# Kernel tuning notes

Hardware: AMD Instinct MI355X
Metric: run time of the kernel (lower is better)

Reference implementation:

```python
import jax, jax.numpy as jnp
import numpy as np

N_NODES = 100000
N_EDGES = 1600000
NODE_IN = 6
EDGE_IN = 4
HID = 128


def _glorot(key, shape):
    fan_in, fan_out = shape[0], shape[1]
    lim = (6.0 / (fan_in + fan_out)) ** 0.5
    return jax.random.uniform(key, shape, jnp.float32, -lim, lim)


def setup_inputs() -> dict:
    key = jax.random.key(0)
    ks = jax.random.split(key, 16)
    x = jax.random.normal(ks[0], (N_NODES, NODE_IN), jnp.float32)
    edge_index = jax.random.randint(ks[1], (2, N_EDGES), 0, N_NODES, jnp.int64)
    edge_attr = jax.random.normal(ks[2], (N_EDGES, EDGE_IN), jnp.float32)
    # SAGEConv params: out = x @ W_root + mean_neigh @ W_neigh + b
    params = {
        "w1_root": _glorot(ks[3], (NODE_IN, HID)),
        "w1_neigh": _glorot(ks[4], (NODE_IN, HID)),
        "b1": jnp.zeros((HID,), jnp.float32),
        "w2_root": _glorot(ks[5], (HID, HID)),
        "w2_neigh": _glorot(ks[6], (HID, HID)),
        "b2": jnp.zeros((HID,), jnp.float32),
        "w_e1": _glorot(ks[7], (2 * HID + EDGE_IN, HID)),
        "b_e1": jnp.zeros((HID,), jnp.float32),
        "w_e2": _glorot(ks[8], (HID, HID // 2)),
        "b_e2": jnp.zeros((HID // 2,), jnp.float32),
        "w_e3": _glorot(ks[9], (HID // 2, 1)),
        "b_e3": jnp.zeros((1,), jnp.float32),
    }
    return {"x": x, "edge_index": edge_index, "edge_attr": edge_attr, **params}


def _sage(x, src, dst, w_root, w_neigh, b):
    # mean aggregation of source features into destination nodes
    agg = jax.ops.segment_sum(x[src], dst, num_segments=N_NODES)
    cnt = jax.ops.segment_sum(jnp.ones((src.shape[0], 1), x.dtype), dst, num_segments=N_NODES)
    mean = agg / jnp.maximum(cnt, 1.0)
    return x @ w_root + mean @ w_neigh + b


def reference(x, edge_index, edge_attr,
              w1_root, w1_neigh, b1, w2_root, w2_neigh, b2,
              w_e1, b_e1, w_e2, b_e2, w_e3, b_e3):
    src, dst = edge_index[0], edge_index[1]
    h = jax.nn.relu(_sage(x, src, dst, w1_root, w1_neigh, b1))
    # dropout is identity in eval mode
    h = jax.nn.relu(_sage(h, src, dst, w2_root, w2_neigh, b2))
    # per-edge representation: [h[src], h[dst], edge_attr] -> MLP -> scalar
    e = jnp.concatenate([h[src], h[dst], edge_attr], axis=-1)  # [E, 2H+Ein]
    e = jax.nn.relu(e @ w_e1 + b_e1)
    e = jax.nn.relu(e @ w_e2 + b_e2)
    out = (e @ w_e3 + b_e3).squeeze(-1)  # [E]
    return out
```

## Files before the change

kernel.cpp:

```cpp
#include <hip/hip_runtime.h>
#include <hip/hip_bf16.h>
#include <stdint.h>


typedef unsigned short u16;
typedef short bf16x8 __attribute__((ext_vector_type(8)));
typedef float f32x4 __attribute__((ext_vector_type(4)));
typedef float f32x2 __attribute__((ext_vector_type(2)));

#define NMASK 0x1FFFF

__device__ __forceinline__ u16 f2b(float f) {
  unsigned u = __builtin_bit_cast(unsigned, f);
  u = u + 0x7fffu + ((u >> 16) & 1u);
  return (u16)(u >> 16);
}
__device__ __forceinline__ float bflo(unsigned u) {
  return __builtin_bit_cast(float, u << 16);
}
__device__ __forceinline__ float bfhi(unsigned u) {
  return __builtin_bit_cast(float, u & 0xffff0000u);
}
__device__ __forceinline__ f32x2 unpk2(unsigned u) {
  return (f32x2){bflo(u), bfhi(u)};
}
__device__ __forceinline__ unsigned pack2bf(float a, float b) {
  unsigned ua = __builtin_bit_cast(unsigned, a);
  unsigned ub = __builtin_bit_cast(unsigned, b);
  ua = ua + 0x7fffu + ((ua >> 16) & 1u);
  ub = ub + 0x7fffu + ((ub >> 16) & 1u);
  return (ua >> 16) | (ub & 0xffff0000u);
}
__device__ __forceinline__ unsigned packrn(f32x2 f) {
  __hip_bfloat162 h = __float22bfloat162_rn(make_float2(f.x, f.y));
  unsigned r;
  __builtin_memcpy(&r, &h, 4);
  return r;
}

__global__ void hist_kernel(const int* __restrict__ ei, int* __restrict__ cnt,
                            int E) {
  int e = blockIdx.x * blockDim.x + threadIdx.x;
  if (e < E) atomicAdd(&cnt[ei[E + e]], 1);
}

__global__ void scan_block_sums(const int* __restrict__ cnt,
                                int* __restrict__ partial, int N) {
  __shared__ int red[256];
  int t = threadIdx.x;
  int n = blockIdx.x * 256 + t;
  red[t] = (n < N) ? cnt[n] : 0;
  __syncthreads();
  for (int off = 128; off; off >>= 1) {
    if (t < off) red[t] += red[t + off];
    __syncthreads();
  }
  if (t == 0) partial[blockIdx.x] = red[0];
}

__global__ void scan_partials(int* __restrict__ partial,
                              int* __restrict__ rowptr, int NBLK, int E,
                              int N) {
  __shared__ int sc[512];
  int t = threadIdx.x;
  int v = (t < NBLK) ? partial[t] : 0;
  sc[t] = v;
  __syncthreads();
  for (int off = 1; off < 512; off <<= 1) {
    int a = (t >= off) ? sc[t - off] : 0;
    __syncthreads();
    sc[t] += a;
    __syncthreads();
  }
  if (t < NBLK) partial[t] = sc[t] - v;
  if (t == 0) rowptr[N] = E;
}

__global__ void scan_final(const int* __restrict__ partial,
                           int* __restrict__ cursor, int* __restrict__ rowptr,
                           int N) {
  __shared__ int sc[256];
  int t = threadIdx.x;
  int n = blockIdx.x * 256 + t;
  int v = (n < N) ? cursor[n] : 0;
  sc[t] = v;
  __syncthreads();
  for (int off = 1; off < 256; off <<= 1) {
    int a = (t >= off) ? sc[t - off] : 0;
    __syncthreads();
    sc[t] += a;
    __syncthreads();
  }
  int excl = partial[blockIdx.x] + sc[t] - v;
  if (n < N) {
    rowptr[n] = excl;
    cursor[n] = excl;
  }
}

__global__ void scatter_rec(const int* __restrict__ ei,
                            const float* __restrict__ attr,
                            int* __restrict__ cursor, uint4* __restrict__ rec,
                            unsigned* __restrict__ src4, int E) {
  int e = blockIdx.x * blockDim.x + threadIdx.x;
  if (e >= E) return;
  int s = ei[e];
  int d = ei[E + e];
  float4 a4 = *(const float4*)(attr + (size_t)e * 4);
  int pos = atomicAdd(&cursor[d], 1);
  uint4 r;
  r.x = (unsigned)s | ((unsigned)(d & 0x7FFF) << 17);
  r.y = ((unsigned)d >> 15) | ((unsigned)e << 2);
  r.z = pack2bf(a4.x, a4.y);
  r.w = pack2bf(a4.z, a4.w);
  rec[pos] = r;
  src4[pos] = (unsigned)s;
}

__global__ void pack_weights(const float* __restrict__ w2_root,
                             const float* __restrict__ w2_neigh,
                             const float* __restrict__ w_e1,
                             const float* __restrict__ w_e2,
                             const float* __restrict__ b_e1,
                             u16* __restrict__ B2f, u16* __restrict__ WSDf,
                             u16* __restrict__ W2f, float* __restrict__ pbias) {
  int t = blockIdx.x * 256 + threadIdx.x;
  if (t < 32768) {
    int j = t & 7, lane = (t >> 3) & 63, nt = (t >> 9) & 7, kt = t >> 12;
    int k = kt * 32 + (lane >> 4) * 8 + j;
    int n = nt * 16 + (lane & 15);
    float v = (k < 128) ? w2_root[k * 128 + n] : w2_neigh[(k - 128) * 128 + n];
    B2f[t] = f2b(v);
  } else if (t < 65536) {
    int t2 = t - 32768;
    int j = t2 & 7, lane = (t2 >> 3) & 63, nt = (t2 >> 9) & 15, kt = t2 >> 13;
    int k = kt * 32 + (lane >> 4) * 8 + j;
    int n = nt * 16 + (lane & 15);
    float v = (n < 128) ? w_e1[k * 128 + n] : w_e1[(128 + k) * 128 + (n - 128)];
    WSDf[t2] = f2b(v);
  } else if (t < 73728) {
    int t2 = t - 65536;
    int j = t2 & 7, lane = (t2 >> 3) & 63, nt = (t2 >> 9) & 3, kt = t2 >> 11;
    int k = kt * 32 + (lane >> 4) * 8 + j;
    int n = nt * 16 + (lane & 15);
    W2f[t2] = f2b(w_e2[k * 64 + n]);
  } else if (t < 73984) {
    int n = t - 73728;
    pbias[n] = (n < 128) ? 0.0f : b_e1[n - 128];
  }
}

__global__ __launch_bounds__(256) void agg1_kernel(
    const float* __restrict__ x, const int* __restrict__ rowptr,
    const unsigned* __restrict__ src4, float* __restrict__ mean1, int N) {
  int n = blockIdx.x * 4 + (threadIdx.x >> 6);
  if (n >= N) return;
  int lane = threadIdx.x & 63;
  int g = lane >> 3;
  int c = lane & 7;
  int beg = rowptr[n], end = rowptr[n + 1];
  float a = 0.0f;
  if (c < 6) {
    int idx[4];
#pragma unroll
    for (int j = 0; j < 4; j++) {
      int ii = beg + g + j * 8;
      idx[j] = (ii < end) ? (int)src4[ii] : -1;
    }
    float v[4];
#pragma unroll
    for (int j = 0; j < 4; j++)
      v[j] = x[(size_t)(idx[j] < 0 ? 0 : idx[j]) * 6 + c];
#pragma unroll
    for (int j = 0; j < 4; j++)
      if (idx[j] >= 0) a += v[j];
    for (int ii = beg + g + 32; ii < end; ii += 8) {
      a += x[(size_t)src4[ii] * 6 + c];
    }
  }
  a += __shfl_xor(a, 8, 64);
  a += __shfl_xor(a, 16, 64);
  a += __shfl_xor(a, 32, 64);
  if (g == 0 && c < 6)
    mean1[(size_t)n * 6 + c] = a / (float)max(end - beg, 1);
}

__global__ __launch_bounds__(256) void dense1_kernel(
    const float* __restrict__ x, const float* __restrict__ mean1,
    const float* __restrict__ w_root, const float* __restrict__ w_neigh,
    const float* __restrict__ b, u16* __restrict__ cat2b, int N) {
  __shared__ float sxm[384];
  int t = threadIdx.x;
  int col = t & 127;
  int half = t >> 7;
  float wr[6], wn[6];
#pragma unroll
  for (int j = 0; j < 6; j++) {
    wr[j] = w_root[j * 128 + col];
    wn[j] = w_neigh[j * 128 + col];
  }
  float bb = b[col];
  for (int base = blockIdx.x * 32; base < N; base += gridDim.x * 32) {
    int cnt = min(32, N - base) * 6;
    __syncthreads();
    for (int i = t; i < 384; i += 256) {
      if (i < 192)
        sxm[i] = (i < cnt) ? x[(size_t)base * 6 + i] : 0.0f;
      else
        sxm[i] = (i - 192 < cnt) ? mean1[(size_t)base * 6 + (i - 192)] : 0.0f;
    }
    __syncthreads();
#pragma unroll
    for (int sub = 0; sub < 16; sub++) {
      int nl = sub * 2 + half;
      int n = base + nl;
      if (n < N) {
        float s = bb;
#pragma unroll
        for (int j = 0; j < 6; j++)
          s += sxm[nl * 6 + j] * wr[j] + sxm[192 + nl * 6 + j] * wn[j];
        cat2b[(size_t)n * 256 + col] = f2b(fmaxf(s, 0.0f));
      }
    }
  }
}

__global__ __launch_bounds__(256) void agg2_kernel(
    const u16* __restrict__ cat2b, u16* __restrict__ cat2w,
    const int* __restrict__ rowptr, const unsigned* __restrict__ src4, int N) {
  int n = blockIdx.x * 4 + (threadIdx.x >> 6);
  if (n >= N) return;
  int lane = threadIdx.x & 63;
  int g = lane >> 4;
  int c = lane & 15;
  int beg = rowptr[n], end = rowptr[n + 1];
  f32x2 acc2[4];
#pragma unroll
  for (int j = 0; j < 4; j++) acc2[j] = (f32x2){0.f, 0.f};

  const int DEPTH = 8;
  int idx[DEPTH];
#pragma unroll
  for (int j = 0; j < DEPTH; j++) {
    int ii = beg + g + j * 4;
    idx[j] = (ii < end) ? (int)src4[ii] : -1;
  }
  uint4 u[DEPTH];
#pragma unroll
  for (int j = 0; j < DEPTH; j++) {
    int s = idx[j] < 0 ? 0 : idx[j];
    u[j] = *(const uint4*)(cat2b + (size_t)s * 256 + c * 8);
  }
#pragma unroll
  for (int j = 0; j < DEPTH; j++) {
    if (idx[j] >= 0) {
      acc2[0] += unpk2(u[j].x);
      acc2[1] += unpk2(u[j].y);
      acc2[2] += unpk2(u[j].z);
      acc2[3] += unpk2(u[j].w);
    }
  }
  for (int ii = beg + g + DEPTH * 4; ii < end; ii += 4) {
    uint4 uu = *(const uint4*)(cat2b + (size_t)src4[ii] * 256 + c * 8);
    acc2[0] += unpk2(uu.x);
    acc2[1] += unpk2(uu.y);
    acc2[2] += unpk2(uu.z);
    acc2[3] += unpk2(uu.w);
  }
#pragma unroll
  for (int j = 0; j < 4; j++) {
    acc2[j].x += __shfl_xor(acc2[j].x, 16, 64);
    acc2[j].y += __shfl_xor(acc2[j].y, 16, 64);
    acc2[j].x += __shfl_xor(acc2[j].x, 32, 64);
    acc2[j].y += __shfl_xor(acc2[j].y, 32, 64);
  }
  if (g == 0) {
    float inv = 1.0f / (float)max(end - beg, 1);
    uint4 ov;
    ov.x = packrn(acc2[0] * inv);
    ov.y = packrn(acc2[1] * inv);
    ov.z = packrn(acc2[2] * inv);
    ov.w = packrn(acc2[3] * inv);
    *(uint4*)(cat2w + (size_t)n * 256 + 128 + c * 8) = ov;
  }
}

template <int KT, int NT, bool RELU>
__global__ __launch_bounds__(512) void mfma_gemm(
    const u16* __restrict__ A, int lda, const u16* __restrict__ Bf,
    const float* __restrict__ bias, u16* __restrict__ C, int ldc, int M) {
  __shared__ u16 sB[KT * NT * 512];
  int tid = threadIdx.x;
  for (int i = tid; i < KT * NT * 64; i += 512)
    ((uint4*)sB)[i] = ((const uint4*)Bf)[i];
  int w = tid >> 6, l = tid & 63;
  int quad = l >> 4, col16 = l & 15;
  int rowA = blockIdx.x * 128 + w * 16 + col16;
  bool rv = rowA < M;
  const u16* ap = A + (size_t)rowA * lda + quad * 8;
  f32x4 acc[NT];
#pragma unroll
  for (int nt = 0; nt < NT; nt++) acc[nt] = (f32x4){0.f, 0.f, 0.f, 0.f};
  __syncthreads();
#pragma unroll
  for (int kt = 0; kt < KT; kt++) {
    bf16x8 av = {};
    if (rv) av = *(const bf16x8*)(ap + kt * 32);
#pragma unroll
    for (int nt = 0; nt < NT; nt++) {
      bf16x8 bv = *(const bf16x8*)(sB + ((kt * NT + nt) * 64 + l) * 8);
      acc[nt] = __builtin_amdgcn_mfma_f32_16x16x32_bf16(av, bv, acc[nt], 0, 0, 0);
    }
  }
  int rowbase = blockIdx.x * 128 + w * 16 + quad * 4;
#pragma unroll
  for (int r = 0; r < 4; r++) {
    int row = rowbase + r;
    if (row < M) {
#pragma unroll
      for (int nt = 0; nt < NT; nt++) {
        float v = acc[nt][r] + bias[nt * 16 + col16];
        if (RELU) v = fmaxf(v, 0.0f);
        C[(size_t)row * ldc + nt * 16 + col16] = f2b(v);
      }
    }
  }
}

__global__ __launch_bounds__(256) void edge_mfma_kernel(
    const u16* __restrict__ Pcatb, const uint4* __restrict__ rec,
    const u16* __restrict__ W2f, const float* __restrict__ b_e2,
    const float* __restrict__ w_e3, const float* __restrict__ b_e3,
    const float* __restrict__ w_e1, float* __restrict__ out, int E) {
  __shared__ u16 sV[64 * 136];
  __shared__ u16 sW2[8192];

  int tid = threadIdx.x;
  int w = tid >> 6, l = tid & 63, quad = l >> 4, c16 = l & 15;
  int egrp = tid >> 4, ac16 = tid & 15;

  for (int i = tid; i < 1024; i += 256)
    ((uint4*)sW2)[i] = ((const uint4*)W2f)[i];

  f32x2 wa2[4][4];
#pragma unroll
  for (int j = 0; j < 4; j++) {
    float4 w0 = *(const float4*)(w_e1 + (256 + j) * 128 + ac16 * 8);
    float4 w1 = *(const float4*)(w_e1 + (256 + j) * 128 + ac16 * 8 + 4);
    wa2[j][0] = (f32x2){w0.x, w0.y};
    wa2[j][1] = (f32x2){w0.z, w0.w};
    wa2[j][2] = (f32x2){w1.x, w1.y};
    wa2[j][3] = (f32x2){w1.z, w1.w};
  }
  float w3v[4], be2[4];
#pragma unroll
  for (int nt = 0; nt < 4; nt++) {
    w3v[nt] = w_e3[nt * 16 + c16];
    be2[nt] = b_e2[nt * 16 + c16];
  }
  float b3 = b_e3[0];

  int tiles = (E + 63) >> 6;
  int S = gridDim.x;

  uint4 rc[4];
  uint4 ps[4], pd[4];
  int eidr[4];

  auto load_rec = [&](int t) {
#pragma unroll
    for (int it = 0; it < 4; it++) {
      int e = min(t * 64 + it * 16 + egrp, E - 1);
      rc[it] = rec[e];
    }
  };
  auto issue_gather = [&]() {
#pragma unroll
    for (int it = 0; it < 4; it++) {
      int s = (int)(rc[it].x & NMASK);
      int d = (int)(((rc[it].x >> 17) | (rc[it].y << 15)) & NMASK);
      eidr[it] = (int)(rc[it].y >> 2);
      ps[it] = *(const uint4*)(Pcatb + (size_t)s * 256 + ac16 * 8);
      pd[it] = *(const uint4*)(Pcatb + (size_t)d * 256 + 128 + ac16 * 8);
    }
  };

  int t = blockIdx.x;
  uint4 rcn[4];
  if (t < tiles) {
    load_rec(t);
    issue_gather();
    if (t + S < tiles) {
#pragma unroll
      for (int it = 0; it < 4; it++) {
        int e = min((t + S) * 64 + it * 16 + egrp, E - 1);
        rcn[it] = rec[e];
      }
    }
  }
  for (; t < tiles; t += S) {
#pragma unroll
    for (int it = 0; it < 4; it++) {
      int e = it * 16 + egrp;
      uint4 psu = ps[it], pdu = pd[it];
      f32x2 a01 = unpk2(rc[it].z);
      f32x2 a23 = unpk2(rc[it].w);
      unsigned pu[4] = {psu.x, psu.y, psu.z, psu.w};
      unsigned du[4] = {pdu.x, pdu.y, pdu.z, pdu.w};
      uint4 ov;
      unsigned* op = (unsigned*)&ov;
#pragma unroll
      for (int p2 = 0; p2 < 4; p2++) {
        f32x2 f = unpk2(pu[p2]) + unpk2(du[p2]);
        f += a01.x * wa2[0][p2];
        f += a01.y * wa2[1][p2];
        f += a23.x * wa2[2][p2];
        f += a23.y * wa2[3][p2];
        f = __builtin_elementwise_max(f, (f32x2){0.f, 0.f});
        op[p2] = packrn(f);
      }
      *(uint4*)(sV + e * 136 + ac16 * 8) = ov;
      if (ac16 == 0) *(unsigned*)(sV + e * 136 + 128) = (unsigned)eidr[it];
    }
    if (t + S < tiles) {
#pragma unroll
      for (int it = 0; it < 4; it++) rc[it] = rcn[it];
      issue_gather();
      if (t + 2 * S < tiles) {
#pragma unroll
        for (int it = 0; it < 4; it++) {
          int e = min((t + 2 * S) * 64 + it * 16 + egrp, E - 1);
          rcn[it] = rec[e];
        }
      }
    }
    __syncthreads();
    f32x4 acc[4];
#pragma unroll
    for (int nt = 0; nt < 4; nt++) acc[nt] = (f32x4){0.f, 0.f, 0.f, 0.f};
    const u16* vp = sV + (w * 16 + c16) * 136 + quad * 8;
#pragma unroll
    for (int kt = 0; kt < 4; kt++) {
      bf16x8 av = *(const bf16x8*)(vp + kt * 32);
#pragma unroll
      for (int nt = 0; nt < 4; nt++) {
        bf16x8 bv = *(const bf16x8*)(sW2 + ((kt * 4 + nt) * 64 + l) * 8);
        acc[nt] = __builtin_amdgcn_mfma_f32_16x16x32_bf16(av, bv, acc[nt], 0, 0, 0);
      }
    }
#pragma unroll
    for (int r = 0; r < 4; r++) {
      float p = 0.0f;
#pragma unroll
      for (int nt = 0; nt < 4; nt++)
        p += fmaxf(acc[nt][r] + be2[nt], 0.0f) * w3v[nt];
      p += __shfl_xor(p, 1, 64);
      p += __shfl_xor(p, 2, 64);
      p += __shfl_xor(p, 4, 64);
      p += __shfl_xor(p, 8, 64);
      if (c16 == 0) {
        int eloc = w * 16 + quad * 4 + r;
        if (t * 64 + eloc < E) {
          unsigned eid = *(const unsigned*)(sV + eloc * 136 + 128);
          out[eid] = p + b3;
        }
      }
    }
    __syncthreads();
  }
}

extern "C" void kernel_launch(void* const* d_in, const int* in_sizes, int n_in,
                              void* d_out, int out_size, void* d_ws,
                              size_t ws_size, hipStream_t stream) {
  const float* x        = (const float*)d_in[0];
  const int*   ei       = (const int*)d_in[1];
  const float* attr     = (const float*)d_in[2];
  const float* w1_root  = (const float*)d_in[3];
  const float* w1_neigh = (const float*)d_in[4];
  const float* b1       = (const float*)d_in[5];
  const float* w2_root  = (const float*)d_in[6];
  const float* w2_neigh = (const float*)d_in[7];
  const float* b2       = (const float*)d_in[8];
  const float* w_e1     = (const float*)d_in[9];
  const float* b_e1     = (const float*)d_in[10];
  const float* w_e2     = (const float*)d_in[11];
  const float* b_e2     = (const float*)d_in[12];
  const float* w_e3     = (const float*)d_in[13];
  const float* b_e3     = (const float*)d_in[14];
  float* out = (float*)d_out;

  int N = in_sizes[0] / 6;
  int E = in_sizes[2] / 4;
  int NBLK = (N + 255) / 256;

  int* wsi = (int*)d_ws;
  int*      rowptr  = wsi;
  int*      cursor  = wsi + 100004;
  int*      partial = wsi + 200004;
  unsigned* src4    = (unsigned*)(wsi + 200516);
  uint4*    rec     = (uint4*)(wsi + 1800520);
  float*    mean1   = (float*)(wsi + 8200520);
  u16*      cat2b   = (u16*)(wsi + 8800520);
  u16*      h2b     = (u16*)(wsi + 21600520);
  u16*      B2f     = (u16*)(wsi + 28000520);
  u16*      WSDf    = (u16*)(wsi + 28016904);
  u16*      W2f     = (u16*)(wsi + 28033288);
  float*    pbias   = (float*)(wsi + 28037384);

  (void)hipMemsetAsync(cursor, 0, (size_t)N * sizeof(int), stream);

  pack_weights<<<289, 256, 0, stream>>>(w2_root, w2_neigh, w_e1, w_e2, b_e1,
                                        B2f, WSDf, W2f, pbias);

  hist_kernel<<<(E + 255) / 256, 256, 0, stream>>>(ei, cursor, E);
  scan_block_sums<<<NBLK, 256, 0, stream>>>(cursor, partial, N);
  scan_partials<<<1, 512, 0, stream>>>(partial, rowptr, NBLK, E, N);
  scan_final<<<NBLK, 256, 0, stream>>>(partial, cursor, rowptr, N);
  scatter_rec<<<(E + 255) / 256, 256, 0, stream>>>(ei, attr, cursor, rec,
                                                   src4, E);

  agg1_kernel<<<(N + 3) / 4, 256, 0, stream>>>(x, rowptr, src4, mean1, N);
  dense1_kernel<<<1024, 256, 0, stream>>>(x, mean1, w1_root, w1_neigh, b1,
                                          cat2b, N);

  agg2_kernel<<<(N + 3) / 4, 256, 0, stream>>>(cat2b, cat2b, rowptr, src4, N);

  int gblocks = (N + 127) / 128;
  mfma_gemm<8, 8, true><<<gblocks, 512, 0, stream>>>(cat2b, 256, B2f, b2, h2b,
                                                     128, N);
  mfma_gemm<4, 16, false><<<gblocks, 512, 0, stream>>>(h2b, 128, WSDf, pbias,
                                                       cat2b, 256, N);

  edge_mfma_kernel<<<1024, 256, 0, stream>>>(cat2b, rec, W2f, b_e2, w_e3,
                                             b_e3, w_e1, out, E);
}
```

Measured before the change: 595.9 us.

## Partition edge records into source-node buckets for cache-local gathers in edge MLP

Adds a stable counting-sort pass (count, scan, scatter) that groups the dst-sorted edge records into 8 buckets by source-node range. Each edge block then handles one bucket, with blockIdx mod 8 selecting it. Within a bucket the source-row gathers from the node projection table touch only about an eighth of the nodes, which should improve L2 hit rates. In exchange it adds three kernels, an extra read and write of 25.6MB of records, and per-bucket load balance that depends on the source distribution.

```diff
diff --git a/kernel.cpp b/kernel.cpp
--- a/kernel.cpp
+++ b/kernel.cpp
@@ -115,6 +115,98 @@
   r.w = pack2bf(a4.z, a4.w);
   rec[pos] = r;
   src4[pos] = (unsigned)s;
+}
+
+__global__ void part_count(const unsigned* __restrict__ src4,
+                           int* __restrict__ bcnt, int E, int NPB,
+                           unsigned bdiv) {
+  __shared__ int h[8];
+  int t = threadIdx.x;
+  if (t < 8) h[t] = 0;
+  __syncthreads();
+  int base = blockIdx.x * 2048 + t * 8;
+#pragma unroll
+  for (int j = 0; j < 8; j++) {
+    int i = base + j;
+    if (i < E) atomicAdd(&h[src4[i] / bdiv], 1);
+  }
+  __syncthreads();
+  if (t < 8) bcnt[t * NPB + blockIdx.x] = h[t];
+}
+
+__global__ void part_scan(int* __restrict__ bcnt, int* __restrict__ bB, int M,
+                          int NPB, int E) {
+  __shared__ int ls[256];
+  int t = threadIdx.x;
+  int chunk = (M + 255) >> 8;
+  int s = 0;
+  for (int j = 0; j < chunk; j++) {
+    int i = t * chunk + j;
+    if (i < M) s += bcnt[i];
+  }
+  ls[t] = s;
+  __syncthreads();
+  for (int off = 1; off < 256; off <<= 1) {
+    int a = (t >= off) ? ls[t - off] : 0;
+    __syncthreads();
+    ls[t] += a;
+    __syncthreads();
+  }
+  int run = ls[t] - s;
+  for (int j = 0; j < chunk; j++) {
+    int i = t * chunk + j;
+    if (i < M) {
+      int v = bcnt[i];
+      bcnt[i] = run;
+      run += v;
+    }
+  }
+  __syncthreads();
+  if (t < 8) bB[t] = bcnt[t * NPB];
+  if (t == 8) bB[8] = E;
+}
+
+__global__ __launch_bounds__(256) void part_scatter(
+    const uint4* __restrict__ rec, const unsigned* __restrict__ src4,
+    const int* __restrict__ bcnt, uint4* __restrict__ rec2, int E, int NPB,
+    unsigned bdiv) {
+  __shared__ int ofs[8][256];
+  int t = threadIdx.x;
+  int base = blockIdx.x * 2048 + t * 8;
+  uint4 r[8];
+  int bk[8];
+  int cnt[8] = {0, 0, 0, 0, 0, 0, 0, 0};
+#pragma unroll
+  for (int j = 0; j < 8; j++) {
+    int i = base + j;
+    if (i < E) {
+      r[j] = rec[i];
+      int b = (int)(src4[i] / bdiv);
+      bk[j] = b;
+      cnt[b]++;
+    } else {
+      bk[j] = -1;
+    }
+  }
+#pragma unroll
+  for (int b = 0; b < 8; b++) ofs[b][t] = cnt[b];
+  __syncthreads();
+  for (int b = 0; b < 8; b++) {
+    for (int off = 1; off < 256; off <<= 1) {
+      int a = (t >= off) ? ofs[b][t - off] : 0;
+      __syncthreads();
+      ofs[b][t] += a;
+      __syncthreads();
+    }
+  }
+  int pos[8];
+#pragma unroll
+  for (int b = 0; b < 8; b++)
+    pos[b] = bcnt[b * NPB + blockIdx.x] + ofs[b][t] - cnt[b];
+#pragma unroll
+  for (int j = 0; j < 8; j++) {
+    if (bk[j] >= 0) rec2[pos[bk[j]]++] = r[j];
+  }
 }
 
 __global__ void pack_weights(const float* __restrict__ w2_root,
@@ -328,10 +420,11 @@
 }
 
 __global__ __launch_bounds__(256) void edge_mfma_kernel(
-    const u16* __restrict__ Pcatb, const uint4* __restrict__ rec,
-    const u16* __restrict__ W2f, const float* __restrict__ b_e2,
-    const float* __restrict__ w_e3, const float* __restrict__ b_e3,
-    const float* __restrict__ w_e1, float* __restrict__ out, int E) {
+    const u16* __restrict__ Pcatb, const uint4* __restrict__ rec2,
+    const int* __restrict__ bB, const u16* __restrict__ W2f,
+    const float* __restrict__ b_e2, const float* __restrict__ w_e3,
+    const float* __restrict__ b_e3, const float* __restrict__ w_e1,
+    float* __restrict__ out) {
   __shared__ u16 sV[64 * 136];
   __shared__ u16 sW2[8192];
 
@@ -360,18 +453,20 @@
   }
   float b3 = b_e3[0];
 
-  int tiles = (E + 63) >> 6;
-  int S = gridDim.x;
-
-  uint4 rc[4];
+  int bucket = blockIdx.x & 7;
+  int bBeg = bB[bucket], bEnd = bB[bucket + 1];
+  int tiles = (bEnd - bBeg + 63) >> 6;
+  int S = gridDim.x >> 3;
+
+  uint4 rc[4], rcn[4];
   uint4 ps[4], pd[4];
   int eidr[4];
 
-  auto load_rec = [&](int t) {
+  auto load_rc = [&](int t, uint4* dst) {
 #pragma unroll
     for (int it = 0; it < 4; it++) {
-      int e = min(t * 64 + it * 16 + egrp, E - 1);
-      rc[it] = rec[e];
+      int e = min(bBeg + t * 64 + it * 16 + egrp, bEnd - 1);
+      dst[it] = rec2[e];
     }
   };
   auto issue_gather = [&]() {
@@ -385,18 +480,11 @@
     }
   };
 
-  int t = blockIdx.x;
-  uint4 rcn[4];
+  int t = blockIdx.x >> 3;
   if (t < tiles) {
-    load_rec(t);
+    load_rc(t, rc);
     issue_gather();
-    if (t + S < tiles) {
-#pragma unroll
-      for (int it = 0; it < 4; it++) {
-        int e = min((t + S) * 64 + it * 16 + egrp, E - 1);
-        rcn[it] = rec[e];
-      }
-    }
+    if (t + S < tiles) load_rc(t + S, rcn);
   }
   for (; t < tiles; t += S) {
 #pragma unroll
@@ -426,13 +514,7 @@
 #pragma unroll
       for (int it = 0; it < 4; it++) rc[it] = rcn[it];
       issue_gather();
-      if (t + 2 * S < tiles) {
-#pragma unroll
-        for (int it = 0; it < 4; it++) {
-          int e = min((t + 2 * S) * 64 + it * 16 + egrp, E - 1);
-          rcn[it] = rec[e];
-        }
-      }
+      if (t + 2 * S < tiles) load_rc(t + 2 * S, rcn);
     }
     __syncthreads();
     f32x4 acc[4];
@@ -460,7 +542,7 @@
       p += __shfl_xor(p, 8, 64);
       if (c16 == 0) {
         int eloc = w * 16 + quad * 4 + r;
-        if (t * 64 + eloc < E) {
+        if (bBeg + t * 64 + eloc < bEnd) {
           unsigned eid = *(const unsigned*)(sV + eloc * 136 + 128);
           out[eid] = p + b3;
         }
@@ -493,6 +575,8 @@
   int N = in_sizes[0] / 6;
   int E = in_sizes[2] / 4;
   int NBLK = (N + 255) / 256;
+  int NPB = (E + 2047) / 2048;
+  unsigned bdiv = (unsigned)((N + 7) / 8);
 
   int* wsi = (int*)d_ws;
   int*      rowptr  = wsi;
@@ -507,6 +591,9 @@
   u16*      WSDf    = (u16*)(wsi + 28016904);
   u16*      W2f     = (u16*)(wsi + 28033288);
   float*    pbias   = (float*)(wsi + 28037384);
+  int*      bcnt    = wsi + 28037640;
+  int*      bB      = wsi + 28043896;
+  uint4*    rec2    = (uint4*)(wsi + 28043908);
 
   (void)hipMemsetAsync(cursor, 0, (size_t)N * sizeof(int), stream);
 
@@ -520,6 +607,10 @@
   scatter_rec<<<(E + 255) / 256, 256, 0, stream>>>(ei, attr, cursor, rec,
                                                    src4, E);
 
+  part_count<<<NPB, 256, 0, stream>>>(src4, bcnt, E, NPB, bdiv);
+  part_scan<<<1, 256, 0, stream>>>(bcnt, bB, 8 * NPB, NPB, E);
+  part_scatter<<<NPB, 256, 0, stream>>>(rec, src4, bcnt, rec2, E, NPB, bdiv);
+
   agg1_kernel<<<(N + 3) / 4, 256, 0, stream>>>(x, rowptr, src4, mean1, N);
   dense1_kernel<<<1024, 256, 0, stream>>>(x, mean1, w1_root, w1_neigh, b1,
                                           cat2b, N);
@@ -532,6 +623,6 @@
   mfma_gemm<4, 16, false><<<gblocks, 512, 0, stream>>>(h2b, 128, WSDf, pbias,
                                                        cat2b, 256, N);
 
-  edge_mfma_kernel<<<1024, 256, 0, stream>>>(cat2b, rec, W2f, b_e2, w_e3,
-                                             b_e3, w_e1, out, E);
-}
+  edge_mfma_kernel<<<1024, 256, 0, stream>>>(cat2b, rec2, bB, W2f, b_e2, w_e3,
+                                             b_e3, w_e1, out);
+}
```

Measured after the change: 655.3 us. +10.0%, slower.

## Bucket edges by source range and assign buckets to XCCs for L2 locality

Applied to the files above, without the earlier changes.

Edges are now sorted into eight buckets by source-node range, then by destination within each bucket, using a second histogram, scan and scatter over an 8×N count array. The edge kernel reads the XCC id, starts on the bucket matching its XCC and takes tiles dynamically through per-bucket atomic counters. The aim is for each XCC's L2 to hold only its slice of source rows, so the random h[src] gathers hit cache more often. In exchange it adds scan passes over 800K counters, a larger memset, extra atomics in the scatter step, and per-tile atomic and barrier overhead in the edge kernel.

```diff
diff --git a/kernel.cpp b/kernel.cpp
--- a/kernel.cpp
+++ b/kernel.cpp
@@ -38,18 +38,22 @@
   return r;
 }
 
-__global__ void hist_kernel(const int* __restrict__ ei, int* __restrict__ cnt,
-                            int E) {
+__global__ void hist_both(const int* __restrict__ ei, int* __restrict__ cnt_d,
+                          int* __restrict__ cnt_bd, int E, int N, int bdiv) {
   int e = blockIdx.x * blockDim.x + threadIdx.x;
-  if (e < E) atomicAdd(&cnt[ei[E + e]], 1);
+  if (e >= E) return;
+  int s = ei[e];
+  int d = ei[E + e];
+  atomicAdd(&cnt_d[d], 1);
+  atomicAdd(&cnt_bd[(size_t)(s / bdiv) * N + d], 1);
 }
 
 __global__ void scan_block_sums(const int* __restrict__ cnt,
-                                int* __restrict__ partial, int N) {
+                                int* __restrict__ partial, int M) {
   __shared__ int red[256];
   int t = threadIdx.x;
   int n = blockIdx.x * 256 + t;
-  red[t] = (n < N) ? cnt[n] : 0;
+  red[t] = (n < M) ? cnt[n] : 0;
   __syncthreads();
   for (int off = 128; off; off >>= 1) {
     if (t < off) red[t] += red[t + off];
@@ -58,27 +62,39 @@
   if (t == 0) partial[blockIdx.x] = red[0];
 }
 
-__global__ void scan_partials(int* __restrict__ partial,
-                              int* __restrict__ rowptr, int NBLK, int E,
-                              int N) {
-  __shared__ int sc[512];
+__global__ void scan_mid(int* __restrict__ partial, int* __restrict__ bB,
+                         int NBLK, int E, int setBB) {
+  __shared__ int ls[256];
   int t = threadIdx.x;
-  int v = (t < NBLK) ? partial[t] : 0;
-  sc[t] = v;
+  int chunk = (NBLK + 255) >> 8;
+  int s = 0;
+  for (int j = 0; j < chunk; j++) {
+    int i = t * chunk + j;
+    if (i < NBLK) s += partial[i];
+  }
+  ls[t] = s;
   __syncthreads();
-  for (int off = 1; off < 512; off <<= 1) {
-    int a = (t >= off) ? sc[t - off] : 0;
-    __syncthreads();
-    sc[t] += a;
-    __syncthreads();
-  }
-  if (t < NBLK) partial[t] = sc[t] - v;
-  if (t == 0) rowptr[N] = E;
+  for (int off = 1; off < 256; off <<= 1) {
+    int a = (t >= off) ? ls[t - off] : 0;
+    __syncthreads();
+    ls[t] += a;
+    __syncthreads();
+  }
+  int run = ls[t] - s;
+  for (int j = 0; j < chunk; j++) {
+    int i = t * chunk + j;
+    if (i < NBLK) {
+      int v = partial[i];
+      partial[i] = run;
+      run += v;
+    }
+  }
+  if (setBB && t == 0) bB[8] = E;
 }
 
 __global__ void scan_final(const int* __restrict__ partial,
                            int* __restrict__ cursor, int* __restrict__ rowptr,
-                           int N) {
+                           int N, int E) {
   __shared__ int sc[256];
   int t = threadIdx.x;
   int n = blockIdx.x * 256 + t;
@@ -96,25 +112,50 @@
     rowptr[n] = excl;
     cursor[n] = excl;
   }
-}
-
-__global__ void scatter_rec(const int* __restrict__ ei,
-                            const float* __restrict__ attr,
-                            int* __restrict__ cursor, uint4* __restrict__ rec,
-                            unsigned* __restrict__ src4, int E) {
+  if (n == 0) rowptr[N] = E;
+}
+
+__global__ void scan_final_bd(const int* __restrict__ partial,
+                              int* __restrict__ cur, int* __restrict__ bB,
+                              int M, int N) {
+  __shared__ int sc[256];
+  int t = threadIdx.x;
+  int n = blockIdx.x * 256 + t;
+  int v = (n < M) ? cur[n] : 0;
+  sc[t] = v;
+  __syncthreads();
+  for (int off = 1; off < 256; off <<= 1) {
+    int a = (t >= off) ? sc[t - off] : 0;
+    __syncthreads();
+    sc[t] += a;
+    __syncthreads();
+  }
+  int excl = partial[blockIdx.x] + sc[t] - v;
+  if (n < M) {
+    cur[n] = excl;
+    if (n - (n / N) * N == 0) bB[n / N] = excl;
+  }
+}
+
+__global__ void scatter_both(const int* __restrict__ ei,
+                             const float* __restrict__ attr,
+                             int* __restrict__ cursor, int* __restrict__ cur_bd,
+                             unsigned* __restrict__ src4,
+                             uint4* __restrict__ rec2, int E, int N, int bdiv) {
   int e = blockIdx.x * blockDim.x + threadIdx.x;
   if (e >= E) return;
   int s = ei[e];
   int d = ei[E + e];
   float4 a4 = *(const float4*)(attr + (size_t)e * 4);
-  int pos = atomicAdd(&cursor[d], 1);
+  int p1 = atomicAdd(&cursor[d], 1);
+  src4[p1] = (unsigned)s;
+  int p2 = atomicAdd(&cur_bd[(size_t)(s / bdiv) * N + d], 1);
   uint4 r;
   r.x = (unsigned)s | ((unsigned)(d & 0x7FFF) << 17);
   r.y = ((unsigned)d >> 15) | ((unsigned)e << 2);
   r.z = pack2bf(a4.x, a4.y);
   r.w = pack2bf(a4.z, a4.w);
-  rec[pos] = r;
-  src4[pos] = (unsigned)s;
+  rec2[p2] = r;
 }
 
 __global__ void pack_weights(const float* __restrict__ w2_root,
@@ -328,12 +369,14 @@
 }
 
 __global__ __launch_bounds__(256) void edge_mfma_kernel(
-    const u16* __restrict__ Pcatb, const uint4* __restrict__ rec,
+    const u16* __restrict__ Pcatb, const uint4* __restrict__ rec2,
+    const int* __restrict__ bB, int* __restrict__ tilecnt,
     const u16* __restrict__ W2f, const float* __restrict__ b_e2,
     const float* __restrict__ w_e3, const float* __restrict__ b_e3,
-    const float* __restrict__ w_e1, float* __restrict__ out, int E) {
+    const float* __restrict__ w_e1, float* __restrict__ out) {
   __shared__ u16 sV[64 * 136];
   __shared__ u16 sW2[8192];
+  __shared__ int sTile;
 
   int tid = threadIdx.x;
   int w = tid >> 6, l = tid & 63, quad = l >> 4, c16 = l & 15;
@@ -360,113 +403,121 @@
   }
   float b3 = b_e3[0];
 
-  int tiles = (E + 63) >> 6;
-  int S = gridDim.x;
-
-  uint4 rc[4];
+  unsigned xcc;
+  asm volatile("s_getreg_b32 %0, hwreg(HW_REG_XCC_ID)" : "=s"(xcc));
+
+  uint4 rc[4], rcn[4];
   uint4 ps[4], pd[4];
   int eidr[4];
 
-  auto load_rec = [&](int t) {
-#pragma unroll
-    for (int it = 0; it < 4; it++) {
-      int e = min(t * 64 + it * 16 + egrp, E - 1);
-      rc[it] = rec[e];
-    }
-  };
-  auto issue_gather = [&]() {
-#pragma unroll
-    for (int it = 0; it < 4; it++) {
-      int s = (int)(rc[it].x & NMASK);
-      int d = (int)(((rc[it].x >> 17) | (rc[it].y << 15)) & NMASK);
-      eidr[it] = (int)(rc[it].y >> 2);
-      ps[it] = *(const uint4*)(Pcatb + (size_t)s * 256 + ac16 * 8);
-      pd[it] = *(const uint4*)(Pcatb + (size_t)d * 256 + 128 + ac16 * 8);
-    }
-  };
-
-  int t = blockIdx.x;
-  uint4 rcn[4];
-  if (t < tiles) {
-    load_rec(t);
+  for (int bb = 0; bb < 8; bb++) {
+    int bucket = (int)((xcc + (unsigned)bb) & 7u);
+    int bBeg = bB[bucket], bEnd = bB[bucket + 1];
+    int tiles = (bEnd - bBeg + 63) >> 6;
+    int* tc = &tilecnt[bucket * 16];
+
+    auto load_rc = [&](int t, uint4* dst) {
+#pragma unroll
+      for (int it = 0; it < 4; it++) {
+        int e = min(bBeg + t * 64 + it * 16 + egrp, bEnd - 1);
+        dst[it] = rec2[e];
+      }
+    };
+    auto issue_gather = [&]() {
+#pragma unroll
+      for (int it = 0; it < 4; it++) {
+        int s = (int)(rc[it].x & NMASK);
+        int d = (int)(((rc[it].x >> 17) | (rc[it].y << 15)) & NMASK);
+        eidr[it] = (int)(rc[it].y >> 2);
+        ps[it] = *(const uint4*)(Pcatb + (size_t)s * 256 + ac16 * 8);
+        pd[it] = *(const uint4*)(Pcatb + (size_t)d * 256 + 128 + ac16 * 8);
+      }
+    };
+
+    __syncthreads();
+    if (tid == 0) sTile = atomicAdd(tc, 1);
+    __syncthreads();
+    int tcur = sTile;
+    __syncthreads();
+    if (tid == 0) sTile = atomicAdd(tc, 1);
+    __syncthreads();
+    int tnext = sTile;
+    if (tcur >= tiles) continue;
+
+    load_rc(tcur, rc);
     issue_gather();
-    if (t + S < tiles) {
+    if (tnext < tiles) load_rc(tnext, rcn);
+
+    while (tcur < tiles) {
 #pragma unroll
       for (int it = 0; it < 4; it++) {
-        int e = min((t + S) * 64 + it * 16 + egrp, E - 1);
-        rcn[it] = rec[e];
-      }
-    }
-  }
-  for (; t < tiles; t += S) {
-#pragma unroll
-    for (int it = 0; it < 4; it++) {
-      int e = it * 16 + egrp;
-      uint4 psu = ps[it], pdu = pd[it];
-      f32x2 a01 = unpk2(rc[it].z);
-      f32x2 a23 = unpk2(rc[it].w);
-      unsigned pu[4] = {psu.x, psu.y, psu.z, psu.w};
-      unsigned du[4] = {pdu.x, pdu.y, pdu.z, pdu.w};
-      uint4 ov;
-      unsigned* op = (unsigned*)&ov;
-#pragma unroll
-      for (int p2 = 0; p2 < 4; p2++) {
-        f32x2 f = unpk2(pu[p2]) + unpk2(du[p2]);
-        f += a01.x * wa2[0][p2];
-        f += a01.y * wa2[1][p2];
-        f += a23.x * wa2[2][p2];
-        f += a23.y * wa2[3][p2];
-        f = __builtin_elementwise_max(f, (f32x2){0.f, 0.f});
-        op[p2] = packrn(f);
-      }
-      *(uint4*)(sV + e * 136 + ac16 * 8) = ov;
-      if (ac16 == 0) *(unsigned*)(sV + e * 136 + 128) = (unsigned)eidr[it];
-    }
-    if (t + S < tiles) {
-#pragma unroll
-      for (int it = 0; it < 4; it++) rc[it] = rcn[it];
-      issue_gather();
-      if (t + 2 * S < tiles) {
-#pragma unroll
-        for (int it = 0; it < 4; it++) {
-          int e = min((t + 2 * S) * 64 + it * 16 + egrp, E - 1);
-          rcn[it] = rec[e];
+        int e = it * 16 + egrp;
+        uint4 psu = ps[it], pdu = pd[it];
+        f32x2 a01 = unpk2(rc[it].z);
+        f32x2 a23 = unpk2(rc[it].w);
+        unsigned pu[4] = {psu.x, psu.y, psu.z, psu.w};
+        unsigned du[4] = {pdu.x, pdu.y, pdu.z, pdu.w};
+        uint4 ov;
+        unsigned* op = (unsigned*)&ov;
+#pragma unroll
+        for (int p2 = 0; p2 < 4; p2++) {
+          f32x2 f = unpk2(pu[p2]) + unpk2(du[p2]);
+          f += a01.x * wa2[0][p2];
+          f += a01.y * wa2[1][p2];
+          f += a23.x * wa2[2][p2];
+          f += a23.y * wa2[3][p2];
+          f = __builtin_elementwise_max(f, (f32x2){0.f, 0.f});
+          op[p2] = packrn(f);
         }
-      }
-    }
-    __syncthreads();
-    f32x4 acc[4];
-#pragma unroll
-    for (int nt = 0; nt < 4; nt++) acc[nt] = (f32x4){0.f, 0.f, 0.f, 0.f};
-    const u16* vp = sV + (w * 16 + c16) * 136 + quad * 8;
-#pragma unroll
-    for (int kt = 0; kt < 4; kt++) {
-      bf16x8 av = *(const bf16x8*)(vp + kt * 32);
-#pragma unroll
-      for (int nt = 0; nt < 4; nt++) {
-        bf16x8 bv = *(const bf16x8*)(sW2 + ((kt * 4 + nt) * 64 + l) * 8);
-        acc[nt] = __builtin_amdgcn_mfma_f32_16x16x32_bf16(av, bv, acc[nt], 0, 0, 0);
-      }
-    }
-#pragma unroll
-    for (int r = 0; r < 4; r++) {
-      float p = 0.0f;
-#pragma unroll
-      for (int nt = 0; nt < 4; nt++)
-        p += fmaxf(acc[nt][r] + be2[nt], 0.0f) * w3v[nt];
-      p += __shfl_xor(p, 1, 64);
-      p += __shfl_xor(p, 2, 64);
-      p += __shfl_xor(p, 4, 64);
-      p += __shfl_xor(p, 8, 64);
-      if (c16 == 0) {
-        int eloc = w * 16 + quad * 4 + r;
-        if (t * 64 + eloc < E) {
-          unsigned eid = *(const unsigned*)(sV + eloc * 136 + 128);
-          out[eid] = p + b3;
+        *(uint4*)(sV + e * 136 + ac16 * 8) = ov;
+        if (ac16 == 0) *(unsigned*)(sV + e * 136 + 128) = (unsigned)eidr[it];
+      }
+      bool have_next = (tnext < tiles);
+      if (have_next) {
+#pragma unroll
+        for (int it = 0; it < 4; it++) rc[it] = rcn[it];
+        issue_gather();
+      }
+      if (tid == 0) sTile = atomicAdd(tc, 1);
+      __syncthreads();
+      int tnn = sTile;
+      if (have_next && tnn < tiles) load_rc(tnn, rcn);
+      f32x4 acc[4];
+#pragma unroll
+      for (int nt = 0; nt < 4; nt++) acc[nt] = (f32x4){0.f, 0.f, 0.f, 0.f};
+      const u16* vp = sV + (w * 16 + c16) * 136 + quad * 8;
+#pragma unroll
+      for (int kt = 0; kt < 4; kt++) {
+        bf16x8 av = *(const bf16x8*)(vp + kt * 32);
+#pragma unroll
+        for (int nt = 0; nt < 4; nt++) {
+          bf16x8 bv = *(const bf16x8*)(sW2 + ((kt * 4 + nt) * 64 + l) * 8);
+          acc[nt] =
+              __builtin_amdgcn_mfma_f32_16x16x32_bf16(av, bv, acc[nt], 0, 0, 0);
         }
       }
-    }
-    __syncthreads();
+#pragma unroll
+      for (int r = 0; r < 4; r++) {
+        float p = 0.0f;
+#pragma unroll
+        for (int nt = 0; nt < 4; nt++)
+          p += fmaxf(acc[nt][r] + be2[nt], 0.0f) * w3v[nt];
+        p += __shfl_xor(p, 1, 64);
+        p += __shfl_xor(p, 2, 64);
+        p += __shfl_xor(p, 4, 64);
+        p += __shfl_xor(p, 8, 64);
+        if (c16 == 0) {
+          int eloc = w * 16 + quad * 4 + r;
+          if (bBeg + tcur * 64 + eloc < bEnd) {
+            unsigned eid = *(const unsigned*)(sV + eloc * 136 + 128);
+            out[eid] = p + b3;
+          }
+        }
+      }
+      __syncthreads();
+      tcur = tnext;
+      tnext = tnn;
+    }
   }
 }
 
@@ -493,32 +544,42 @@
   int N = in_sizes[0] / 6;
   int E = in_sizes[2] / 4;
   int NBLK = (N + 255) / 256;
+  int M2 = 8 * N;
+  int NBLK2 = (M2 + 255) / 256;
+  int bdiv = (N + 7) / 8;
 
   int* wsi = (int*)d_ws;
   int*      rowptr  = wsi;
   int*      cursor  = wsi + 100004;
-  int*      partial = wsi + 200004;
-  unsigned* src4    = (unsigned*)(wsi + 200516);
-  uint4*    rec     = (uint4*)(wsi + 1800520);
-  float*    mean1   = (float*)(wsi + 8200520);
-  u16*      cat2b   = (u16*)(wsi + 8800520);
-  u16*      h2b     = (u16*)(wsi + 21600520);
-  u16*      B2f     = (u16*)(wsi + 28000520);
-  u16*      WSDf    = (u16*)(wsi + 28016904);
-  u16*      W2f     = (u16*)(wsi + 28033288);
-  float*    pbias   = (float*)(wsi + 28037384);
-
-  (void)hipMemsetAsync(cursor, 0, (size_t)N * sizeof(int), stream);
+  int*      cur_bd  = wsi + 200004;
+  int*      tilecnt = wsi + 1000004;
+  int*      partial = wsi + 1000132;
+  int*      bB      = wsi + 1004228;
+  unsigned* src4    = (unsigned*)(wsi + 1004240);
+  uint4*    rec2    = (uint4*)(wsi + 2604240);
+  float*    mean1   = (float*)(wsi + 9004240);
+  u16*      cat2b   = (u16*)(wsi + 9604240);
+  u16*      h2b     = (u16*)(wsi + 22404240);
+  u16*      B2f     = (u16*)(wsi + 28804240);
+  u16*      WSDf    = (u16*)(wsi + 28820624);
+  u16*      W2f     = (u16*)(wsi + 28837008);
+  float*    pbias   = (float*)(wsi + 28841104);
+
+  (void)hipMemsetAsync(cursor, 0, (size_t)900128 * sizeof(int), stream);
 
   pack_weights<<<289, 256, 0, stream>>>(w2_root, w2_neigh, w_e1, w_e2, b_e1,
                                         B2f, WSDf, W2f, pbias);
 
-  hist_kernel<<<(E + 255) / 256, 256, 0, stream>>>(ei, cursor, E);
+  hist_both<<<(E + 255) / 256, 256, 0, stream>>>(ei, cursor, cur_bd, E, N,
+                                                 bdiv);
   scan_block_sums<<<NBLK, 256, 0, stream>>>(cursor, partial, N);
-  scan_partials<<<1, 512, 0, stream>>>(partial, rowptr, NBLK, E, N);
-  scan_final<<<NBLK, 256, 0, stream>>>(partial, cursor, rowptr, N);
-  scatter_rec<<<(E + 255) / 256, 256, 0, stream>>>(ei, attr, cursor, rec,
-                                                   src4, E);
+  scan_mid<<<1, 256, 0, stream>>>(partial, bB, NBLK, E, 0);
+  scan_final<<<NBLK, 256, 0, stream>>>(partial, cursor, rowptr, N, E);
+  scan_block_sums<<<NBLK2, 256, 0, stream>>>(cur_bd, partial, M2);
+  scan_mid<<<1, 256, 0, stream>>>(partial, bB, NBLK2, E, 1);
+  scan_final_bd<<<NBLK2, 256, 0, stream>>>(partial, cur_bd, bB, M2, N);
+  scatter_both<<<(E + 255) / 256, 256, 0, stream>>>(ei, attr, cursor, cur_bd,
+                                                    src4, rec2, E, N, bdiv);
 
   agg1_kernel<<<(N + 3) / 4, 256, 0, stream>>>(x, rowptr, src4, mean1, N);
   dense1_kernel<<<1024, 256, 0, stream>>>(x, mean1, w1_root, w1_neigh, b1,
@@ -532,6 +593,6 @@
   mfma_gemm<4, 16, false><<<gblocks, 512, 0, stream>>>(h2b, 128, WSDf, pbias,
                                                        cat2b, 256, N);
 
-  edge_mfma_kernel<<<1024, 256, 0, stream>>>(cat2b, rec, W2f, b_e2, w_e3,
-                                             b_e3, w_e1, out, E);
-}
+  edge_mfma_kernel<<<1024, 256, 0, stream>>>(cat2b, rec2, bB, tilecnt, W2f,
+                                             b_e2, w_e3, b_e3, w_e1, out);
+}
```

After: 832.4 us. +39.7%, slower.
